# Optimization experiments

Measured on AMD Instinct MI355X. Metric: run time of the kernel, lower is better.

The kernel has to match this reference:

```python
import jax, jax.numpy as jnp
import numpy as np


def setup_inputs() -> dict:
    key = jax.random.key(0)
    k_x, k_qkv, k_proj, k_bias = jax.random.split(key, 4)
    b, n, dim = 4, 8192, 512
    h, w = 8, 256
    x = jax.random.normal(k_x, (b, n, dim), dtype=jnp.float32)
    # Linear weights stored as [in, out] (transpose of torch's [out, in])
    Wqkv = jax.random.normal(k_qkv, (dim, 3 * dim), dtype=jnp.float32) * 0.02
    bqkv = jnp.zeros((3 * dim,), dtype=jnp.float32)
    Wproj = jax.random.normal(k_proj, (dim, dim), dtype=jnp.float32) * 0.02
    bproj = jnp.zeros((dim,), dtype=jnp.float32)
    # torch init is zeros; use small randn so the bias path is exercised
    attn_bias = jax.random.normal(k_bias, (h, w, w), dtype=jnp.float32) * 0.02
    return {"x": x, "Wqkv": Wqkv, "bqkv": bqkv, "Wproj": Wproj,
            "bproj": bproj, "attn_bias": attn_bias}


def reference(x, Wqkv, bqkv, Wproj, bproj, attn_bias):
    b, n, c = x.shape
    h, w, _ = attn_bias.shape
    d = c // h
    nw = n // w  # number of non-overlapping windows (n divisible by w)
    qkv = (x @ Wqkv + bqkv).reshape(b, n, 3, h, d)
    q, k, v = jnp.moveaxis(qkv, 2, 0)  # each [b, n, h, d]

    def to_windows(t):
        # [b, n, h, d] -> [b, h, nw, w, d]
        return t.reshape(b, nw, w, h, d).transpose(0, 3, 1, 2, 4)

    q, k, v = to_windows(q), to_windows(k), to_windows(v)
    scale = d ** -0.5
    # block-local attention: [b, h, nw, w, w]
    attn = jnp.einsum('bhnqd,bhnkd->bhnqk', q, k) * scale + attn_bias[None, :, None]
    attn = jax.nn.softmax(attn, axis=-1)
    out = jnp.einsum('bhnqk,bhnkd->bhnqd', attn, v)
    # [b, h, nw, w, d] -> [b, n, h*d]
    out = out.transpose(0, 2, 3, 1, 4).reshape(b, n, c)
    return out @ Wproj + bproj
```

## Files before the change

kernel.cpp:

```cpp
#include <hip/hip_runtime.h>

typedef unsigned short u16;
typedef unsigned int u32;
typedef __bf16 bf16x8 __attribute__((ext_vector_type(8)));
typedef float f32x4 __attribute__((ext_vector_type(4)));


__device__ __forceinline__ u16 f2bf(float f) {
  u32 u = __builtin_bit_cast(u32, f);
  u32 r = (u + 0x7fffu + ((u >> 16) & 1u)) >> 16;
  return (u16)r;
}
__device__ __forceinline__ u32 pk2(float a, float b) {
  return (u32)f2bf(a) | ((u32)f2bf(b) << 16);
}
__device__ __forceinline__ f32x4 mfma16(bf16x8 a, bf16x8 b, f32x4 c) {
  return __builtin_amdgcn_mfma_f32_16x16x32_bf16(a, b, c, 0, 0, 0);
}
__device__ __forceinline__ void glds16(const void* g, void* l) {
  typedef __attribute__((address_space(1))) void as1_void;
  typedef __attribute__((address_space(3))) void as3_void;
  __builtin_amdgcn_global_load_lds((as1_void*)g, (as3_void*)l, 16, 0, 0);
}


__launch_bounds__(256)
__global__ void convert_x_k(const float* __restrict__ in, u16* __restrict__ out) {
  long i = ((long)blockIdx.x * 256 + threadIdx.x) * 8;
  float4 f0 = *(const float4*)(in + i);
  float4 f1 = *(const float4*)(in + i + 4);
  uint4 o;
  o.x = pk2(f0.x, f0.y);
  o.y = pk2(f0.z, f0.w);
  o.z = pk2(f1.x, f1.y);
  o.w = pk2(f1.z, f1.w);
  *(uint4*)(out + i) = o;
}


__launch_bounds__(256)
__global__ void transpose_w_k(const float* __restrict__ in, u16* __restrict__ out,
                              int K, int N) {
  __shared__ float t[32][33];
  int n0 = blockIdx.x * 32, k0 = blockIdx.y * 32;
  int tx = threadIdx.x & 31, ty = threadIdx.x >> 5;
#pragma unroll
  for (int s = 0; s < 32; s += 8)
    t[ty + s][tx] = in[(long)(k0 + ty + s) * N + n0 + tx];
  __syncthreads();
#pragma unroll
  for (int s = 0; s < 32; s += 8)
    out[(long)(n0 + ty + s) * K + k0 + tx] = f2bf(t[tx][ty + s]);
}


__launch_bounds__(256)
__global__ void bias_transform_k(const float* __restrict__ bias, float* __restrict__ biasT) {
  int hb = blockIdx.x;
  int h = hb >> 4, rt = hb & 15;
  int lane = threadIdx.x & 63;
  int quad = lane >> 4, l15 = lane & 15;
  int jtg = threadIdx.x >> 6;
  const float L = 1.44269504f;
#pragma unroll
  for (int i = 0; i < 4; ++i) {
    int jt = jtg * 4 + i;
    float4 v = *(const float4*)&bias[((long)h * 256 + rt * 16 + l15) * 256 + jt * 16 + quad * 4];
    v.x *= L; v.y *= L; v.z *= L; v.w *= L;
    *(float4*)&biasT[(((long)hb * 16 + jt) * 64 + lane) * 4] = v;
  }
}


template <int EPI>
__launch_bounds__(256)
__global__ void gemm_bt(const u16* __restrict__ A, const u16* __restrict__ Bt,
                        const float* __restrict__ bias,
                        u16* __restrict__ oqk, u16* __restrict__ ovt,
                        float* __restrict__ ofp) {
  constexpr int K = 512;
  __shared__ u16 Asm[8192];
  __shared__ u16 Bsm[8192];

  const int tid = threadIdx.x;
  const int wave = tid >> 6, lane = tid & 63;
  const int quad = lane >> 4, l15 = lane & 15;
  const int wm = wave >> 1, wn = wave & 1;
  const int gsw = quad ^ ((l15 >> 1) & 3);
  const long arow0 = (long)blockIdx.y * 128;
  const long brow0 = (long)blockIdx.x * 128;

  f32x4 acc[4][4] = {};

  for (int k0 = 0; k0 < K; k0 += 64) {
#pragma unroll
    for (int rd = 0; rd < 4; ++rd) {
      int flat = rd * 256 + tid;
      int c = flat >> 9, row = (flat >> 2) & 127, gp = flat & 3;
      int g = gp ^ ((row >> 1) & 3);
      const long koff = k0 + c * 32 + g * 8;
      glds16(A + (arow0 + row) * K + koff, &Asm[(rd * 256 + wave * 64) * 8]);
      glds16(Bt + (brow0 + row) * K + koff, &Bsm[(rd * 256 + wave * 64) * 8]);
    }
    __syncthreads();
#pragma unroll
    for (int c = 0; c < 2; ++c) {
      bf16x8 af[4], bfr[4];
#pragma unroll
      for (int i = 0; i < 4; ++i)
        af[i] = *(const bf16x8*)&Asm[c * 4096 + (wm * 64 + i * 16 + l15) * 32 + gsw * 8];
#pragma unroll
      for (int j = 0; j < 4; ++j)
        bfr[j] = *(const bf16x8*)&Bsm[c * 4096 + (wn * 64 + j * 16 + l15) * 32 + gsw * 8];
#pragma unroll
      for (int i = 0; i < 4; ++i)
#pragma unroll
        for (int j = 0; j < 4; ++j)
          acc[i][j] = mfma16(af[i], bfr[j], acc[i][j]);
    }
    __syncthreads();
  }

#pragma unroll
  for (int j = 0; j < 4; ++j) {
    const int C = (int)brow0 + wn * 64 + j * 16 + l15;
    const float bc = bias[C];
#pragma unroll
    for (int i = 0; i < 4; ++i) {
      const long R0 = arow0 + wm * 64 + i * 16 + quad * 4;
      float v4[4];
#pragma unroll
      for (int r = 0; r < 4; ++r) v4[r] = acc[i][j][r] + bc;
      if constexpr (EPI == 0) {
        if (C < 1024) {
#pragma unroll
          for (int r = 0; r < 4; ++r) oqk[(R0 + r) * 1024 + C] = f2bf(v4[r]);
        } else {
          const int hc = (C >> 6) & 7, dc = C & 63;
          const int b = (int)(R0 >> 13), n0 = (int)(R0 & 8191);
          uint2 w;
          w.x = pk2(v4[0], v4[1]);
          w.y = pk2(v4[2], v4[3]);
          *(uint2*)&ovt[((long)(b * 8 + hc) * 64 + dc) * 8192 + n0] = w;
        }
      } else {
#pragma unroll
        for (int r = 0; r < 4; ++r) ofp[(R0 + r) * 512 + C] = v4[r];
      }
    }
  }
}


__launch_bounds__(512, 4)
__global__ void attn_win(const u16* __restrict__ qk, const u16* __restrict__ vtb,
                         const float* __restrict__ biasT, u16* __restrict__ og) {
  __shared__ __align__(16) u16 kS[16384];
  __shared__ __align__(16) u16 vS[16384];
  __shared__ __align__(16) u16 pS[8][1024];

  const int tid = threadIdx.x;
  const int wave = tid >> 6, lane = tid & 63;
  const int quad = lane >> 4, l15 = lane & 15;
  const int gsw = quad ^ ((l15 >> 1) & 3);

  const int wi = blockIdx.x;
  const int nwi = wi & 31, hi = (wi >> 5) & 7, bi = wi >> 8;
  const long grow = (long)bi * 8192 + nwi * 256;
  const u16* qp = qk + grow * 1024 + hi * 64;
  const u16* kp = qp + 512;
  const u16* vp = vtb + (long)(bi * 8 + hi) * 64 * 8192 + nwi * 256;

#pragma unroll
  for (int it = 0; it < 4; ++it) {
    int flat = it * 512 + tid;
    int t = flat >> 3, dg = flat & 7;
    int c = dg >> 2, gp = (dg & 3) ^ ((t >> 1) & 3);
    int4 val = *(const int4*)&kp[(long)t * 1024 + dg * 8];
    *(int4*)&kS[c * 8192 + t * 32 + gp * 8] = val;
  }
#pragma unroll
  for (int it = 0; it < 4; ++it) {
    int flat = it * 512 + tid;
    int d = flat >> 5, tg = flat & 31;
    int kk = tg >> 2, gp = (tg & 3) ^ ((d >> 1) & 3);
    int4 val = *(const int4*)&vp[(long)d * 8192 + tg * 8];
    *(int4*)&vS[kk * 2048 + d * 32 + gp * 8] = val;
  }
  __syncthreads();

  u16* Pw = pS[wave];
  const float cscale = 0.18033688f;

#pragma unroll
  for (int sc = 0; sc < 2; ++sc) {
    const int q0 = wave * 32 + sc * 16;
    const int rt = wave * 2 + sc;
    const float* bT = &biasT[(long)(hi * 16 + rt) * 16 * 64 * 4];

    bf16x8 bq0 = *(const bf16x8*)&qp[(long)(q0 + l15) * 1024 + quad * 8];
    bf16x8 bq1 = *(const bf16x8*)&qp[(long)(q0 + l15) * 1024 + 32 + quad * 8];

    f32x4 sum4 = {0.f, 0.f, 0.f, 0.f};
    f32x4 o[4] = {};

#pragma unroll
    for (int m = 0; m < 4; ++m) {
#pragma unroll
      for (int j2 = 0; j2 < 4; ++j2) {
        const int jt = m * 4 + j2;
        bf16x8 a0 = *(const bf16x8*)&kS[(jt * 16 + l15) * 32 + gsw * 8];
        bf16x8 a1 = *(const bf16x8*)&kS[8192 + (jt * 16 + l15) * 32 + gsw * 8];
        f32x4 z = {0.f, 0.f, 0.f, 0.f};
        z = mfma16(a0, bq0, z);
        z = mfma16(a1, bq1, z);
        f32x4 bb = *(const f32x4*)&bT[(long)jt * 256 + lane * 4];
        f32x4 p;
#pragma unroll
        for (int r = 0; r < 4; ++r) {
          p[r] = __builtin_exp2f(z[r] * cscale + bb[r]);
          sum4[r] += p[r];
        }
        const int gp = ((jt & 1) * 2 + (quad >> 1)) ^ ((l15 >> 1) & 3);
        const int slot = (jt >> 1) & 1;
        uint2 w;
        w.x = pk2(p[0], p[1]);
        w.y = pk2(p[2], p[3]);
        *(uint2*)&Pw[slot * 512 + l15 * 32 + gp * 8 + (quad & 1) * 4] = w;
      }
#pragma unroll
      for (int kk2 = 0; kk2 < 2; ++kk2) {
        const int kk = m * 2 + kk2;
        bf16x8 bp = *(const bf16x8*)&Pw[kk2 * 512 + l15 * 32 + gsw * 8];
#pragma unroll
        for (int dt = 0; dt < 4; ++dt) {
          bf16x8 av = *(const bf16x8*)&vS[kk * 2048 + (dt * 16 + l15) * 32 + gsw * 8];
          o[dt] = mfma16(av, bp, o[dt]);
        }
      }
    }

    float sum = (sum4[0] + sum4[1]) + (sum4[2] + sum4[3]);
    sum += __shfl_xor(sum, 16);
    sum += __shfl_xor(sum, 32);
    const float inv = 1.0f / sum;

    const long rowoff = (grow + q0 + l15) * 512 + hi * 64 + quad * 4;
#pragma unroll
    for (int dt = 0; dt < 4; ++dt) {
      uint2 w;
      w.x = pk2(o[dt][0] * inv, o[dt][1] * inv);
      w.y = pk2(o[dt][2] * inv, o[dt][3] * inv);
      *(uint2*)&og[rowoff + dt * 16] = w;
    }
  }
}


extern "C" void kernel_launch(void* const* d_in, const int* in_sizes, int n_in,
                              void* d_out, int out_size, void* d_ws, size_t ws_size,
                              hipStream_t stream) {
  const float* x     = (const float*)d_in[0];
  const float* Wqkv  = (const float*)d_in[1];
  const float* bqkv  = (const float*)d_in[2];
  const float* Wproj = (const float*)d_in[3];
  const float* bproj = (const float*)d_in[4];
  const float* abias = (const float*)d_in[5];
  float* out = (float*)d_out;

  char* ws = (char*)d_ws;
  u16*   qkp    = (u16*)(ws);
  u16*   vtb    = (u16*)(ws + 67108864L);
  u16*   wqkvT  = (u16*)(ws + 100663296L);
  u16*   wprojT = (u16*)(ws + 102236160L);
  float* biasTp = (float*)(ws + 102760448L);
  u16*   xbf    = (u16*)(ws + 104857600L);
  u16*   attnout = xbf;

  convert_x_k<<<8192, 256, 0, stream>>>(x, xbf);
  transpose_w_k<<<dim3(48, 16), 256, 0, stream>>>(Wqkv, wqkvT, 512, 1536);
  transpose_w_k<<<dim3(16, 16), 256, 0, stream>>>(Wproj, wprojT, 512, 512);
  bias_transform_k<<<128, 256, 0, stream>>>(abias, biasTp);
  gemm_bt<0><<<dim3(12, 256), 256, 0, stream>>>(xbf, wqkvT, bqkv,
                                                qkp, vtb, nullptr);
  attn_win<<<1024, 512, 0, stream>>>(qkp, vtb, biasTp, attnout);
  gemm_bt<1><<<dim3(4, 256), 256, 0, stream>>>(attnout, wprojT, bproj,
                                               nullptr, nullptr, out);
}
```

Measured before the change: 309.4 us.

## Merge prep kernels into one launch and remap blocks for XCD locality

Folds the four preprocessing kernels (x conversion, two weight transposes, bias transform) into one launch dispatched by block id, which cuts launch overhead. The GEMM and attention grids are remapped so that consecutive blocks, which the hardware spreads round-robin across the 8 XCDs, land on the same XCD for related rows and windows, aiming for better L2 reuse. Q fragment loads in attention are hoisted ahead of the K/V staging so their latency overlaps. The remapping assumes round-robin XCD dispatch, and the merged prep kernel now reserves transpose shared memory for every block, including the conversion blocks that do not use it.

```diff
diff --git a/kernel.cpp b/kernel.cpp
--- a/kernel.cpp
+++ b/kernel.cpp
@@ -24,25 +24,10 @@
 }
 
 
-__launch_bounds__(256)
-__global__ void convert_x_k(const float* __restrict__ in, u16* __restrict__ out) {
-  long i = ((long)blockIdx.x * 256 + threadIdx.x) * 8;
-  float4 f0 = *(const float4*)(in + i);
-  float4 f1 = *(const float4*)(in + i + 4);
-  uint4 o;
-  o.x = pk2(f0.x, f0.y);
-  o.y = pk2(f0.z, f0.w);
-  o.z = pk2(f1.x, f1.y);
-  o.w = pk2(f1.z, f1.w);
-  *(uint4*)(out + i) = o;
-}
-
-
-__launch_bounds__(256)
-__global__ void transpose_w_k(const float* __restrict__ in, u16* __restrict__ out,
-                              int K, int N) {
+__device__ __forceinline__ void transpose_body(const float* __restrict__ in,
+                                               u16* __restrict__ out,
+                                               int N, int n0, int k0) {
   __shared__ float t[32][33];
-  int n0 = blockIdx.x * 32, k0 = blockIdx.y * 32;
   int tx = threadIdx.x & 31, ty = threadIdx.x >> 5;
 #pragma unroll
   for (int s = 0; s < 32; s += 8)
@@ -50,34 +35,55 @@
   __syncthreads();
 #pragma unroll
   for (int s = 0; s < 32; s += 8)
-    out[(long)(n0 + ty + s) * K + k0 + tx] = f2bf(t[tx][ty + s]);
-}
-
+    out[(long)(n0 + ty + s) * 512 + k0 + tx] = f2bf(t[tx][ty + s]);
+}
 
 __launch_bounds__(256)
-__global__ void bias_transform_k(const float* __restrict__ bias, float* __restrict__ biasT) {
-  int hb = blockIdx.x;
-  int h = hb >> 4, rt = hb & 15;
-  int lane = threadIdx.x & 63;
-  int quad = lane >> 4, l15 = lane & 15;
-  int jtg = threadIdx.x >> 6;
-  const float L = 1.44269504f;
-#pragma unroll
-  for (int i = 0; i < 4; ++i) {
-    int jt = jtg * 4 + i;
-    float4 v = *(const float4*)&bias[((long)h * 256 + rt * 16 + l15) * 256 + jt * 16 + quad * 4];
-    v.x *= L; v.y *= L; v.z *= L; v.w *= L;
-    *(float4*)&biasT[(((long)hb * 16 + jt) * 64 + lane) * 4] = v;
+__global__ void prep_k(const float* __restrict__ x, u16* __restrict__ xbf,
+                       const float* __restrict__ Wqkv, u16* __restrict__ wqkvT,
+                       const float* __restrict__ Wproj, u16* __restrict__ wprojT,
+                       const float* __restrict__ bias, float* __restrict__ biasT) {
+  const int id = blockIdx.x;
+  if (id < 8192) {
+    long i = ((long)id * 256 + threadIdx.x) * 8;
+    float4 f0 = *(const float4*)(x + i);
+    float4 f1 = *(const float4*)(x + i + 4);
+    uint4 o;
+    o.x = pk2(f0.x, f0.y);
+    o.y = pk2(f0.z, f0.w);
+    o.z = pk2(f1.x, f1.y);
+    o.w = pk2(f1.z, f1.w);
+    *(uint4*)(xbf + i) = o;
+  } else if (id < 8960) {
+    int bx = id - 8192;
+    transpose_body(Wqkv, wqkvT, 1536, (bx % 48) * 32, (bx / 48) * 32);
+  } else if (id < 9216) {
+    int bx = id - 8960;
+    transpose_body(Wproj, wprojT, 512, (bx & 15) * 32, (bx >> 4) * 32);
+  } else {
+    int hb = id - 9216;
+    int h = hb >> 4, rt = hb & 15;
+    int lane = threadIdx.x & 63;
+    int quad = lane >> 4, l15 = lane & 15;
+    int jtg = threadIdx.x >> 6;
+    const float L = 1.44269504f;
+#pragma unroll
+    for (int i = 0; i < 4; ++i) {
+      int jt = jtg * 4 + i;
+      float4 v = *(const float4*)&bias[((long)h * 256 + rt * 16 + l15) * 256 + jt * 16 + quad * 4];
+      v.x *= L; v.y *= L; v.z *= L; v.w *= L;
+      *(float4*)&biasT[(((long)hb * 16 + jt) * 64 + lane) * 4] = v;
+    }
   }
 }
 
 
 template <int EPI>
-__launch_bounds__(256)
-__global__ void gemm_bt(const u16* __restrict__ A, const u16* __restrict__ Bt,
-                        const float* __restrict__ bias,
-                        u16* __restrict__ oqk, u16* __restrict__ ovt,
-                        float* __restrict__ ofp) {
+__device__ __forceinline__ void gemm_body(const u16* __restrict__ A, const u16* __restrict__ Bt,
+                                          const float* __restrict__ bias,
+                                          u16* __restrict__ oqk, u16* __restrict__ ovt,
+                                          float* __restrict__ ofp,
+                                          long arow0, long brow0) {
   constexpr int K = 512;
   __shared__ u16 Asm[8192];
   __shared__ u16 Bsm[8192];
@@ -87,8 +93,6 @@
   const int quad = lane >> 4, l15 = lane & 15;
   const int wm = wave >> 1, wn = wave & 1;
   const int gsw = quad ^ ((l15 >> 1) & 3);
-  const long arow0 = (long)blockIdx.y * 128;
-  const long brow0 = (long)blockIdx.x * 128;
 
   f32x4 acc[4][4] = {};
 
@@ -152,6 +156,28 @@
 }
 
 
+__launch_bounds__(256)
+__global__ void qkv_gemm_k(const u16* __restrict__ A, const u16* __restrict__ Bt,
+                           const float* __restrict__ bias,
+                           u16* __restrict__ oqk, u16* __restrict__ ovt) {
+  int bid = blockIdx.x;
+  int xcd = bid & 7, i = bid >> 3;
+  int nt = i % 12, mtl = i / 12;
+  gemm_body<0>(A, Bt, bias, oqk, ovt, nullptr,
+               (long)(xcd * 32 + mtl) * 128, (long)nt * 128);
+}
+
+__launch_bounds__(256)
+__global__ void proj_gemm_k(const u16* __restrict__ A, const u16* __restrict__ Bt,
+                            const float* __restrict__ bias, float* __restrict__ ofp) {
+  int bid = blockIdx.x;
+  int xcd = bid & 7, i = bid >> 3;
+  int nt = i & 3, mtl = i >> 2;
+  gemm_body<1>(A, Bt, bias, nullptr, nullptr, ofp,
+               (long)(xcd * 32 + mtl) * 128, (long)nt * 128);
+}
+
+
 __launch_bounds__(512, 4)
 __global__ void attn_win(const u16* __restrict__ qk, const u16* __restrict__ vtb,
                          const float* __restrict__ biasT, u16* __restrict__ og) {
@@ -165,11 +191,21 @@
   const int gsw = quad ^ ((l15 >> 1) & 3);
 
   const int wi = blockIdx.x;
-  const int nwi = wi & 31, hi = (wi >> 5) & 7, bi = wi >> 8;
+  const int xcd = wi & 7, hi = (wi >> 3) & 7, wl = wi >> 6;
+  const int win = xcd * 16 + wl;
+  const int nwi = win & 31, bi = win >> 5;
   const long grow = (long)bi * 8192 + nwi * 256;
   const u16* qp = qk + grow * 1024 + hi * 64;
   const u16* kp = qp + 512;
   const u16* vp = vtb + (long)(bi * 8 + hi) * 64 * 8192 + nwi * 256;
+
+  bf16x8 bq[2][2];
+#pragma unroll
+  for (int sc = 0; sc < 2; ++sc) {
+    const int q0 = wave * 32 + sc * 16;
+    bq[sc][0] = *(const bf16x8*)&qp[(long)(q0 + l15) * 1024 + quad * 8];
+    bq[sc][1] = *(const bf16x8*)&qp[(long)(q0 + l15) * 1024 + 32 + quad * 8];
+  }
 
 #pragma unroll
   for (int it = 0; it < 4; ++it) {
@@ -198,9 +234,6 @@
     const int rt = wave * 2 + sc;
     const float* bT = &biasT[(long)(hi * 16 + rt) * 16 * 64 * 4];
 
-    bf16x8 bq0 = *(const bf16x8*)&qp[(long)(q0 + l15) * 1024 + quad * 8];
-    bf16x8 bq1 = *(const bf16x8*)&qp[(long)(q0 + l15) * 1024 + 32 + quad * 8];
-
     f32x4 sum4 = {0.f, 0.f, 0.f, 0.f};
     f32x4 o[4] = {};
 
@@ -212,8 +245,8 @@
         bf16x8 a0 = *(const bf16x8*)&kS[(jt * 16 + l15) * 32 + gsw * 8];
         bf16x8 a1 = *(const bf16x8*)&kS[8192 + (jt * 16 + l15) * 32 + gsw * 8];
         f32x4 z = {0.f, 0.f, 0.f, 0.f};
-        z = mfma16(a0, bq0, z);
-        z = mfma16(a1, bq1, z);
+        z = mfma16(a0, bq[sc][0], z);
+        z = mfma16(a1, bq[sc][1], z);
         f32x4 bb = *(const f32x4*)&bT[(long)jt * 256 + lane * 4];
         f32x4 p;
 #pragma unroll
@@ -277,13 +310,8 @@
   u16*   xbf    = (u16*)(ws + 104857600L);
   u16*   attnout = xbf;
 
-  convert_x_k<<<8192, 256, 0, stream>>>(x, xbf);
-  transpose_w_k<<<dim3(48, 16), 256, 0, stream>>>(Wqkv, wqkvT, 512, 1536);
-  transpose_w_k<<<dim3(16, 16), 256, 0, stream>>>(Wproj, wprojT, 512, 512);
-  bias_transform_k<<<128, 256, 0, stream>>>(abias, biasTp);
-  gemm_bt<0><<<dim3(12, 256), 256, 0, stream>>>(xbf, wqkvT, bqkv,
-                                                qkp, vtb, nullptr);
+  prep_k<<<9344, 256, 0, stream>>>(x, xbf, Wqkv, wqkvT, Wproj, wprojT, abias, biasTp);
+  qkv_gemm_k<<<3072, 256, 0, stream>>>(xbf, wqkvT, bqkv, qkp, vtb);
   attn_win<<<1024, 512, 0, stream>>>(qkp, vtb, biasTp, attnout);
-  gemm_bt<1><<<dim3(4, 256), 256, 0, stream>>>(attnout, wprojT, bproj,
-                                               nullptr, nullptr, out);
-}
+  proj_gemm_k<<<1024, 256, 0, stream>>>(attnout, wprojT, bproj, out);
+}
```

After: 280.9 us. -9.2%, faster.
